# Performance work log

Measured on AMD Instinct MI355X. Metric: run time of the kernel, lower is better.

## Reference

```python
import jax, jax.numpy as jnp
import numpy as np

B, L, D, H, NB = 8, 256, 128, 4, 2
HD = D // H
N_ITEMS, TIME_SPAN = 50000, 256
EPS = 1e-8
NEG = -(2.0 ** 32) + 1.0  # torch uses -2**32+1 padding value


def _ln(x, g, b):
    m = jnp.mean(x, -1, keepdims=True)
    v = jnp.mean((x - m) ** 2, -1, keepdims=True)
    return (x - m) / jnp.sqrt(v + EPS) * g + b


def setup_inputs() -> dict:
    ks = iter(jax.random.split(jax.random.key(0), 40))

    def nrm(shape, s=0.02):
        return jax.random.normal(next(ks), shape, jnp.float32) * s

    inp = {
        "user_ids": jax.random.randint(next(ks), (B,), 0, 1000),
        "log_seqs": jax.random.randint(next(ks), (B, L), 0, N_ITEMS + 1),
        "time_matrices": jax.random.randint(next(ks), (B, L, L), 0, TIME_SPAN + 1),
        "pos_seqs": jax.random.randint(next(ks), (B, L), 1, N_ITEMS + 1),
        "neg_seqs": jax.random.randint(next(ks), (B, L), 1, N_ITEMS + 1),
    }
    inp["item_emb"] = nrm((N_ITEMS + 1, D)).at[0].set(0.0)  # padding_idx=0
    inp["posK_emb"] = nrm((L, D))
    inp["posV_emb"] = nrm((L, D))
    inp["timeK_emb"] = nrm((TIME_SPAN + 1, D))
    inp["timeV_emb"] = nrm((TIME_SPAN + 1, D))
    inp["ln1_g"] = jnp.ones((NB, D)); inp["ln1_b"] = jnp.zeros((NB, D))
    inp["Wq"] = nrm((NB, D, D)); inp["bq"] = jnp.zeros((NB, D))
    inp["Wk"] = nrm((NB, D, D)); inp["bk"] = jnp.zeros((NB, D))
    inp["Wv"] = nrm((NB, D, D)); inp["bv"] = jnp.zeros((NB, D))
    inp["ln2_g"] = jnp.ones((NB, D)); inp["ln2_b"] = jnp.zeros((NB, D))
    inp["W1"] = nrm((NB, D, D)); inp["b1"] = jnp.zeros((NB, D))
    inp["W2"] = nrm((NB, D, D)); inp["b2"] = jnp.zeros((NB, D))
    inp["lnf_g"] = jnp.ones((D,)); inp["lnf_b"] = jnp.zeros((D,))
    return inp


def reference(user_ids, log_seqs, time_matrices, pos_seqs, neg_seqs,
              item_emb, posK_emb, posV_emb, timeK_emb, timeV_emb,
              ln1_g, ln1_b, Wq, bq, Wk, bk, Wv, bv, ln2_g, ln2_b,
              W1, b1, W2, b2, lnf_g, lnf_b):
    # dropout layers are identity in eval mode
    seqs = item_emb[log_seqs] * jnp.sqrt(jnp.float32(D))          # [B,L,D]
    tK = timeK_emb[time_matrices].reshape(B, L, L, H, HD)          # [B,Lq,Lk,H,hd]
    tV = timeV_emb[time_matrices].reshape(B, L, L, H, HD)
    pad = log_seqs == 0                                            # [B,L]
    seqs = seqs * (~pad)[..., None]
    causal = jnp.triu(jnp.ones((L, L), bool), 1)                   # ~tril -> masked
    # time_mask masks by QUERY position (matches torch unsqueeze(-1).expand)
    mask = pad[:, None, :, None] | causal[None, None]              # [B,1,Lq,Lk]
    posKh = posK_emb.reshape(L, H, HD)
    posVh = posV_emb.reshape(L, H, HD)
    for i in range(NB):
        q_in = _ln(seqs, ln1_g[i], ln1_b[i])
        Qh = (q_in @ Wq[i] + bq[i]).reshape(B, L, H, HD).transpose(0, 2, 1, 3)
        Kh = (seqs @ Wk[i] + bk[i]).reshape(B, L, H, HD).transpose(0, 2, 1, 3)
        Vh = (seqs @ Wv[i] + bv[i]).reshape(B, L, H, HD).transpose(0, 2, 1, 3)
        scores = jnp.einsum("bhqd,bhkd->bhqk", Qh, Kh)
        scores = scores + jnp.einsum("bhqd,khd->bhqk", Qh, posKh)
        scores = scores + jnp.einsum("bqkhd,bhqd->bhqk", tK, Qh)
        scores = scores / jnp.sqrt(jnp.float32(HD))
        scores = jnp.where(mask, NEG, scores)
        A = jax.nn.softmax(scores, axis=-1)                        # [B,H,Lq,Lk]
        out = jnp.einsum("bhqk,bhkd->bhqd", A, Vh)
        out = out + jnp.einsum("bhqk,khd->bhqd", A, posVh)
        out = out + jnp.einsum("bhqk,bqkhd->bhqd", A, tV)
        out = out.transpose(0, 2, 1, 3).reshape(B, L, D)
        seqs = q_in + out                                          # residual on Q
        seqs = _ln(seqs, ln2_g[i], ln2_b[i])
        h = jax.nn.relu(seqs @ W1[i] + b1[i])                      # conv1d k=1 == linear
        seqs = seqs + (h @ W2[i] + b2[i])
        seqs = seqs * (~pad)[..., None]
    feats = _ln(seqs, lnf_g, lnf_b)
    pos_logits = jnp.sum(feats * item_emb[pos_seqs], -1)           # [B,L]
    neg_logits = jnp.sum(feats * item_emb[neg_seqs], -1)
    return (pos_logits, neg_logits)
```

## Files before the change

kernel.cpp:

```cpp
#include <hip/hip_runtime.h>
#include <hip/hip_bf16.h>

#define L_ 256
#define H_ 4
#define ROWS 2048
#define NEGV (-4294967295.0f)

typedef unsigned short us16;

__device__ __forceinline__ float us2f(us16 u){ return __uint_as_float(((unsigned)u)<<16); }
__device__ __forceinline__ us16 f2us(float f){ __hip_bfloat16 h=__float2bfloat16(f); return *(us16*)&h; }

__device__ __forceinline__ float dot2bf(unsigned x, unsigned y, float c){
#if __has_builtin(__builtin_amdgcn_fdot2_f32_bf16)
    typedef __bf16 bf2 __attribute__((ext_vector_type(2)));
    union U{ unsigned u; bf2 v; };
    U ux, uy; ux.u=x; uy.u=y;
    return __builtin_amdgcn_fdot2_f32_bf16(ux.v, uy.v, c, false);
#else
    float r=fmaf(us2f((us16)(x&0xffffu)), us2f((us16)(y&0xffffu)), c);
    return fmaf(us2f((us16)(x>>16)), us2f((us16)(y>>16)), r);
#endif
}

struct KArgs {
    const int *log_seqs, *tmat, *pos_seqs, *neg_seqs;
    const float *item_emb, *posK, *posV, *timeK, *timeV;
    const float *ln1g, *ln1b, *bq, *bk, *bv, *ln2g, *ln2b, *b1, *b2, *lnfg, *lnfb;
    const float *Wq, *Wk, *Wv, *W1, *W2;
    float *qin0, *qin1, *out;
    unsigned *wsP;
    us16 *tmK, *tmV, *Qb0, *Kb0, *Vb0, *Qb1, *Kb1, *Vb1;
};

__device__ __forceinline__ void ln_rows(float* sA,
        const float* __restrict__ g, const float* __restrict__ b,
        float* qin_out, int r0, int tid){
    int r=tid>>5, l=tid&31;
    float* x=sA+r*128;
    float x0=x[l],x1=x[l+32],x2=x[l+64],x3=x[l+96];
    float s=x0+x1+x2+x3;
    #pragma unroll
    for(int o=16;o;o>>=1) s+=__shfl_xor(s,o,64);
    float m=s*(1.f/128.f);
    float d0=x0-m,d1=x1-m,d2=x2-m,d3=x3-m;
    float v=d0*d0+d1*d1+d2*d2+d3*d3;
    #pragma unroll
    for(int o=16;o;o>>=1) v+=__shfl_xor(v,o,64);
    float rstd=rsqrtf(v*(1.f/128.f)+1e-8f);
    float y0=d0*rstd*g[l]+b[l];
    float y1=d1*rstd*g[l+32]+b[l+32];
    float y2=d2*rstd*g[l+64]+b[l+64];
    float y3=d3*rstd*g[l+96]+b[l+96];
    x[l]=y0; x[l+32]=y1; x[l+64]=y2; x[l+96]=y3;
    if(qin_out){
        float* q=qin_out+(size_t)(r0+r)*128;
        q[l]=y0; q[l+32]=y1; q[l+64]=y2; q[l+96]=y3;
    }
}

__device__ __forceinline__ float gemv128(const unsigned* __restrict__ wp,
                                         const unsigned* __restrict__ xp, int c){
    float s0=0.f, s1=0.f;
    #pragma unroll 8
    for(int kp=0;kp<64;kp+=2){
        s0=dot2bf(xp[kp],   wp[kp*128+c],     s0);
        s1=dot2bf(xp[kp+1], wp[(kp+1)*128+c], s1);
    }
    return s0+s1;
}

__global__ __launch_bounds__(256) void k_pre(KArgs a){
    __shared__ __align__(16) float sA[1024];
    int tid=threadIdx.x, bid=blockIdx.x;
    if(bid<768){
        int m=bid>>8, rg=bid&255, r0=rg*8;
        {
            int rl=tid>>5, c4=tid&31;
            int id=a.log_seqs[r0+rl];
            float4 v=((const float4*)a.item_emb)[id*32+c4];
            float sc = id? 11.3137085f : 0.f;
            v.x*=sc; v.y*=sc; v.z*=sc; v.w*=sc;
            ((float4*)sA)[tid]=v;
        }
        __syncthreads();
        if(m==0){ ln_rows(sA, a.ln1g, a.ln1b, a.qin0, r0, tid); __syncthreads(); }
        const float* Wsrc=(m==0)?a.Wq:(m==1)?a.Wk:a.Wv;
        int cp=tid&63, rp=tid>>6, c0=2*cp, ra=2*rp, rb=ra+1;
        float a00=0,a01=0,a10=0,a11=0;
        const float* Ar=sA+ra*128;
        const float* Br=sA+rb*128;
        #pragma unroll 8
        for(int kk=0;kk<128;kk++){
            float2 wp=((const float2*)(Wsrc+(size_t)kk*128))[cp];
            float x0=Ar[kk], x1=Br[kk];
            a00=fmaf(x0,wp.x,a00); a01=fmaf(x0,wp.y,a01);
            a10=fmaf(x1,wp.x,a10); a11=fmaf(x1,wp.y,a11);
        }
        int r_a=r0+ra, r_b=r0+rb;
        if(m==0){
            float b0v=a.bq[c0], b1v=a.bq[c0+1];
            ushort2 s0; s0.x=f2us(a00+b0v); s0.y=f2us(a01+b1v);
            ushort2 s1; s1.x=f2us(a10+b0v); s1.y=f2us(a11+b1v);
            *(ushort2*)(a.Qb0+(size_t)r_a*128+c0)=s0;
            *(ushort2*)(a.Qb0+(size_t)r_b*128+c0)=s1;
        } else if(m==1){
            float b0v=a.bk[c0], b1v=a.bk[c0+1];
            int qa=r_a&255, qb2=r_b&255;
            ushort2 s0; s0.x=f2us(a00+b0v+a.posK[qa*128+c0]);  s0.y=f2us(a01+b1v+a.posK[qa*128+c0+1]);
            ushort2 s1; s1.x=f2us(a10+b0v+a.posK[qb2*128+c0]); s1.y=f2us(a11+b1v+a.posK[qb2*128+c0+1]);
            *(ushort2*)(a.Kb0+(size_t)r_a*128+c0)=s0;
            *(ushort2*)(a.Kb0+(size_t)r_b*128+c0)=s1;
        } else {
            float b0v=a.bv[c0], b1v=a.bv[c0+1];
            int qa=r_a&255, qb2=r_b&255;
            unsigned lo0=f2us(a00+b0v+a.posV[qa*128+c0]);
            unsigned lo1=f2us(a01+b1v+a.posV[qa*128+c0+1]);
            unsigned hi0=f2us(a10+b0v+a.posV[qb2*128+c0]);
            unsigned hi1=f2us(a11+b1v+a.posV[qb2*128+c0+1]);
            unsigned* Vo=(unsigned*)a.Vb0+((size_t)r_a>>1)*128;
            Vo[c0]  =lo0|(hi0<<16);
            Vo[c0+1]=lo1|(hi1<<16);
        }
    } else if(bid<880){
        int j=bid-768; int m=j>>4; int sub=j&15;
        const float* base;
        switch(m){
            case 0: base=a.W1; break;        case 1: base=a.W2; break;
            case 2: base=a.Wq+16384; break;  case 3: base=a.Wk+16384; break;
            case 4: base=a.Wv+16384; break;  case 5: base=a.W1+16384; break;
            default: base=a.W2+16384; break;
        }
        unsigned* dst=a.wsP+(size_t)m*8192;
        #pragma unroll
        for(int t2=0;t2<2;t2++){
            int o=sub*512+t2*256+tid;
            int kp=o>>7, c=o&127;
            unsigned lo=f2us(base[(size_t)(2*kp)*128+c]);
            unsigned hi=f2us(base[(size_t)(2*kp+1)*128+c]);
            dst[o]=lo|(hi<<16);
        }
    } else {
        int gi=(bid-880)*256+tid;
        if(gi<8224){
            float4 v=((const float4*)a.timeK)[gi];
            ushort4 o; o.x=f2us(v.x);o.y=f2us(v.y);o.z=f2us(v.z);o.w=f2us(v.w);
            ((ushort4*)a.tmK)[gi]=o;
        } else if(gi<16448){
            int g2=gi-8224;
            float4 v=((const float4*)a.timeV)[g2];
            ushort4 o; o.x=f2us(v.x);o.y=f2us(v.y);o.z=f2us(v.z);o.w=f2us(v.w);
            ((ushort4*)a.tmV)[g2]=o;
        }
    }
}

__global__ __launch_bounds__(256,4) void k_blk(KArgs a, int layer){
    __shared__ __align__(16) float    sS[8*256];
    __shared__ __align__(16) unsigned sAb[8*128];
    __shared__ __align__(16) unsigned sQb[128];
    __shared__ __align__(16) int      sTM[512];
    __shared__ __align__(16) float    sPr[16*128];
    __shared__ float sRed[4], sRed2[4], sRB[8];
    __shared__ __align__(16) float    sX[256];
    __shared__ __align__(16) unsigned sXb[128];
    __shared__ __align__(16) unsigned sHb[128];
    __shared__ __align__(16) unsigned sYb[128];

    int tid=threadIdx.x, bid=blockIdx.x;
    int b=bid>>7, p=bid&127;
    int q1=p, q2=255-p, b0=b*L_;
    int r1=b0+q1, r2=b0+q2;
    bool pad1=a.log_seqs[r1]==0, pad2=a.log_seqs[r2]==0;
    const us16* Qb = layer? a.Qb1:a.Qb0;
    const us16* Kb = layer? a.Kb1:a.Kb0;
    const unsigned* Vbu = (const unsigned*)(layer? a.Vb1:a.Vb0);
    const float* qin = layer? a.qin1:a.qin0;
    const float scale=0.17677669529663687f;

    if(tid<128){
        int rowq=tid>>6, j=tid&63;
        int r=rowq?r2:r1;
        sQb[rowq*64+j]=((const unsigned*)Qb)[(size_t)r*64+j];
    }
    int k=tid;
    int tm1=a.tmat[(size_t)r1*L_+k], tm2=a.tmat[(size_t)r2*L_+k];
    sTM[k]=tm1; sTM[256+k]=tm2;
    __syncthreads();

    {
        const uint4* K4=(const uint4*)(Kb+(size_t)(b0+k)*128);
        #pragma unroll
        for(int i2=0;i2<2;i2++){
            int qq=i2?q2:q1; bool pad=i2?pad2:pad1;
            int tm=i2?tm2:tm1;
            bool act=(k<=qq)&&!pad;
            float acc[4]={0.f,0.f,0.f,0.f};
            if(act){
                const uint4* T4=(const uint4*)(a.tmK+(size_t)tm*128);
                const uint4* Q4=(const uint4*)(sQb+i2*64);
                #pragma unroll
                for(int c=0;c<16;c++){
                    uint4 kv=K4[c], tv=T4[c], qv=Q4[c];
                    float t=acc[c>>2];
                    t=dot2bf(qv.x,kv.x,t); t=dot2bf(qv.y,kv.y,t);
                    t=dot2bf(qv.z,kv.z,t); t=dot2bf(qv.w,kv.w,t);
                    t=dot2bf(qv.x,tv.x,t); t=dot2bf(qv.y,tv.y,t);
                    t=dot2bf(qv.z,tv.z,t); t=dot2bf(qv.w,tv.w,t);
                    acc[c>>2]=t;
                }
            }
            #pragma unroll
            for(int h2=0;h2<H_;h2++) sS[(i2*4+h2)*256+k]= act? acc[h2]*scale : NEGV;
        }
    }
    __syncthreads();

    {
        int h=tid>>6, lane=tid&63;
        us16* sab=(us16*)sAb;
        #pragma unroll
        for(int i2=0;i2<2;i2++){
            const float* row=sS+(i2*4+h)*256;
            float v0=row[lane],v1=row[lane+64],v2=row[lane+128],v3=row[lane+192];
            float mm=fmaxf(fmaxf(v0,v1),fmaxf(v2,v3));
            #pragma unroll
            for(int o=32;o;o>>=1) mm=fmaxf(mm,__shfl_xor(mm,o,64));
            float e0=__expf(v0-mm),e1=__expf(v1-mm),e2=__expf(v2-mm),e3=__expf(v3-mm);
            float ss=e0+e1+e2+e3;
            #pragma unroll
            for(int o=32;o;o>>=1) ss+=__shfl_xor(ss,o,64);
            float inv=1.f/ss;
            us16* ar=sab+(i2*4+h)*256;
            ar[lane]    =f2us(e0*inv); ar[lane+64] =f2us(e1*inv);
            ar[lane+128]=f2us(e2*inv); ar[lane+192]=f2us(e3*inv);
        }
    }
    __syncthreads();

    {
        int i2=tid>>7, s8=(tid>>4)&7, dq=tid&15;
        int qq=i2?q2:q1; bool pad=i2?pad2:pad1;
        int kend=pad?L_:qq+1;
        int k0=s8*32;
        int kmax=kend-k0; kmax=kmax<0?0:(kmax>32?32:kmax);
        int npair=(kmax+1)>>1;
        const unsigned* arow=sAb+(i2*4+(dq>>2))*128;
        const int* tmrow=sTM+i2*256;
        float ac0=0,ac1=0,ac2=0,ac3=0,ac4=0,ac5=0,ac6=0,ac7=0;
        for(int kp=0;kp<npair;kp++){
            int kx=k0+2*kp;
            unsigned aa=arow[kx>>1];
            int tma=tmrow[kx], tmb=tmrow[kx+1];
            const uint4* Vp=(const uint4*)(Vbu+((size_t)(b0+kx)>>1)*128+dq*8);
            uint4 va=Vp[0], vb4=Vp[1];
            uint4 ta=((const uint4*)(a.tmV+(size_t)tma*128))[dq];
            uint4 tb=((const uint4*)(a.tmV+(size_t)tmb*128))[dq];
            ac0=dot2bf(aa,va.x,ac0);  ac1=dot2bf(aa,va.y,ac1);
            ac2=dot2bf(aa,va.z,ac2);  ac3=dot2bf(aa,va.w,ac3);
            ac4=dot2bf(aa,vb4.x,ac4); ac5=dot2bf(aa,vb4.y,ac5);
            ac6=dot2bf(aa,vb4.z,ac6); ac7=dot2bf(aa,vb4.w,ac7);
            unsigned p0=__builtin_amdgcn_perm(tb.x,ta.x,0x05040100u);
            unsigned p1=__builtin_amdgcn_perm(tb.x,ta.x,0x07060302u);
            unsigned p2=__builtin_amdgcn_perm(tb.y,ta.y,0x05040100u);
            unsigned p3=__builtin_amdgcn_perm(tb.y,ta.y,0x07060302u);
            unsigned p4=__builtin_amdgcn_perm(tb.z,ta.z,0x05040100u);
            unsigned p5=__builtin_amdgcn_perm(tb.z,ta.z,0x07060302u);
            unsigned p6=__builtin_amdgcn_perm(tb.w,ta.w,0x05040100u);
            unsigned p7=__builtin_amdgcn_perm(tb.w,ta.w,0x07060302u);
            ac0=dot2bf(aa,p0,ac0); ac1=dot2bf(aa,p1,ac1);
            ac2=dot2bf(aa,p2,ac2); ac3=dot2bf(aa,p3,ac3);
            ac4=dot2bf(aa,p4,ac4); ac5=dot2bf(aa,p5,ac5);
            ac6=dot2bf(aa,p6,ac6); ac7=dot2bf(aa,p7,ac7);
        }
        float* dst=sPr+(i2*8+s8)*128+dq*8;
        ((float4*)dst)[0]=make_float4(ac0,ac1,ac2,ac3);
        ((float4*)dst)[1]=make_float4(ac4,ac5,ac6,ac7);
    }
    __syncthreads();

    int ii=tid>>7, l=tid&127;
    bool padown = ii? pad2:pad1;
    int rr = ii? r2:r1;
    int qown = ii? q2:q1;
    {
        float v=qin[(size_t)rr*128+l];
        #pragma unroll
        for(int sl=0;sl<8;sl++) v+=sPr[(ii*8+sl)*128+l];
        float s=v;
        #pragma unroll
        for(int o=32;o;o>>=1) s+=__shfl_xor(s,o,64);
        if((tid&63)==0) sRed[ii*2+((tid>>6)&1)]=s;
        __syncthreads();
        float m=(sRed[ii*2]+sRed[ii*2+1])*(1.f/128.f);
        float d=v-m;
        float vv=d*d;
        #pragma unroll
        for(int o=32;o;o>>=1) vv+=__shfl_xor(vv,o,64);
        if((tid&63)==0) sRed2[ii*2+((tid>>6)&1)]=vv;
        __syncthreads();
        float rstd=rsqrtf((sRed2[ii*2]+sRed2[ii*2+1])*(1.f/128.f)+1e-8f);
        float y=d*rstd*a.ln2g[layer*128+l]+a.ln2b[layer*128+l];
        sX[ii*128+l]=y;
        ((us16*)sXb)[ii*128+l]=f2us(y);
    }
    __syncthreads();

    int cc=l;
    {
        const unsigned* W1p=a.wsP+(size_t)(layer?5:0)*8192;
        float h1=gemv128(W1p, sXb+ii*64, cc);
        h1=fmaxf(h1+a.b1[layer*128+cc],0.f);
        ((us16*)sHb)[ii*128+cc]=f2us(h1);
    }
    __syncthreads();
    float f;
    {
        const unsigned* W2p=a.wsP+(size_t)(layer?6:1)*8192;
        f=gemv128(W2p, sHb+ii*64, cc)+a.b2[layer*128+cc]+sX[ii*128+cc];
        if(padown) f=0.f;
    }

    if(layer==0){
        ((us16*)sYb)[ii*128+cc]=f2us(f);
        float s=f;
        #pragma unroll
        for(int o=32;o;o>>=1) s+=__shfl_xor(s,o,64);
        if((tid&63)==0) sRB[ii*2+((tid>>6)&1)]=s;
        __syncthreads();
        float m=(sRB[ii*2]+sRB[ii*2+1])*(1.f/128.f);
        float d=f-m;
        float vv=d*d;
        #pragma unroll
        for(int o=32;o;o>>=1) vv+=__shfl_xor(vv,o,64);
        if((tid&63)==0) sRB[4+ii*2+((tid>>6)&1)]=vv;
        __syncthreads();
        float rstd=rsqrtf((sRB[4+ii*2]+sRB[5+ii*2])*(1.f/128.f)+1e-8f);
        float y1=d*rstd*a.ln1g[128+cc]+a.ln1b[128+cc];
        a.qin1[(size_t)rr*128+cc]=y1;
        ((us16*)sXb)[ii*128+cc]=f2us(y1);
        __syncthreads();
        float accq=gemv128(a.wsP+(size_t)2*8192, sXb+ii*64, cc)+a.bq[128+cc];
        a.Qb1[(size_t)rr*128+cc]=f2us(accq);
        float acck=gemv128(a.wsP+(size_t)3*8192, sYb+ii*64, cc)+a.bk[128+cc]+a.posK[qown*128+cc];
        a.Kb1[(size_t)rr*128+cc]=f2us(acck);
        float accv=gemv128(a.wsP+(size_t)4*8192, sYb+ii*64, cc)+a.bv[128+cc]+a.posV[qown*128+cc];
        ((us16*)a.Vb1)[((size_t)rr>>1)*256+2*cc+(rr&1)]=f2us(accv);
    } else {
        float s=f;
        #pragma unroll
        for(int o=32;o;o>>=1) s+=__shfl_xor(s,o,64);
        if((tid&63)==0) sRB[ii*2+((tid>>6)&1)]=s;
        __syncthreads();
        float m=(sRB[ii*2]+sRB[ii*2+1])*(1.f/128.f);
        float d=f-m;
        float vv=d*d;
        #pragma unroll
        for(int o=32;o;o>>=1) vv+=__shfl_xor(vv,o,64);
        if((tid&63)==0) sRB[4+ii*2+((tid>>6)&1)]=vv;
        __syncthreads();
        float rstd=rsqrtf((sRB[4+ii*2]+sRB[5+ii*2])*(1.f/128.f)+1e-8f);
        sX[ii*128+cc]=d*rstd*a.lnfg[cc]+a.lnfb[cc];
        __syncthreads();
        int w=tid>>6, lane=tid&63;
        int rowi=w>>1, neg=w&1;
        int rg = rowi? r2:r1;
        int id = neg? a.neg_seqs[rg] : a.pos_seqs[rg];
        const float* e=a.item_emb+(size_t)id*128;
        float s2 = sX[rowi*128+lane]*e[lane] + sX[rowi*128+lane+64]*e[lane+64];
        #pragma unroll
        for(int o=32;o;o>>=1) s2+=__shfl_xor(s2,o,64);
        if(lane==0) a.out[neg*ROWS+rg]=s2;
    }
}

extern "C" void kernel_launch(void* const* d_in, const int* in_sizes, int n_in,
                              void* d_out, int out_size, void* d_ws, size_t ws_size,
                              hipStream_t stream) {
    KArgs a;
    a.log_seqs=(const int*)d_in[1];
    a.tmat    =(const int*)d_in[2];
    a.pos_seqs=(const int*)d_in[3];
    a.neg_seqs=(const int*)d_in[4];
    a.item_emb=(const float*)d_in[5];
    a.posK =(const float*)d_in[6];
    a.posV =(const float*)d_in[7];
    a.timeK=(const float*)d_in[8];
    a.timeV=(const float*)d_in[9];
    a.ln1g=(const float*)d_in[10];
    a.ln1b=(const float*)d_in[11];
    a.Wq=(const float*)d_in[12];
    a.bq=(const float*)d_in[13];
    a.Wk=(const float*)d_in[14];
    a.bk=(const float*)d_in[15];
    a.Wv=(const float*)d_in[16];
    a.bv=(const float*)d_in[17];
    a.ln2g=(const float*)d_in[18];
    a.ln2b=(const float*)d_in[19];
    a.W1=(const float*)d_in[20];
    a.b1=(const float*)d_in[21];
    a.W2=(const float*)d_in[22];
    a.b2=(const float*)d_in[23];
    a.lnfg=(const float*)d_in[24];
    a.lnfb=(const float*)d_in[25];

    const size_t MB=1u<<20;
    char* w=(char*)d_ws;
    a.qin0=(float*)(w+0*MB);
    a.qin1=(float*)(w+1*MB);
    a.Qb0 =(us16*) (w+2*MB);
    a.Kb0 =(us16*) (w+2*MB+512*1024);
    a.Vb0 =(us16*) (w+3*MB);
    a.Qb1 =(us16*) (w+3*MB+512*1024);
    a.Kb1 =(us16*) (w+4*MB);
    a.Vb1 =(us16*) (w+4*MB+512*1024);
    a.wsP =(unsigned*)(w+5*MB);
    a.tmK =(us16*) (w+5*MB+256*1024);
    a.tmV =(us16*) (w+5*MB+384*1024);
    a.out =(float*)d_out;

    k_pre<<<946,256,0,stream>>>(a);
    k_blk<<<1024,256,0,stream>>>(a,0);
    k_blk<<<1024,256,0,stream>>>(a,1);
}
```

Baseline: 203.0 us.

## Precompute query-time-embedding projections and double block threads to 512

The kernel now precomputes Q·timeK dot products for all 257 time buckets once per block. Per-key scoring then looks up this table instead of streaming a timeK row per key, which removes most of the time-embedding gather traffic from the score phase. The block grows from 256 to 512 threads: the PV accumulation is split into 16 key slices and the FFN and projection GEMVs are split over K into halves reduced through shared memory. Shared buffers are aliased into a union to keep LDS usage down. In exchange the kernel has more barriers and idle half-blocks in the layer-norm phases, and 512 threads with launch bounds of 4 blocks may limit registers.

```diff
diff --git a/kernel.cpp b/kernel.cpp
--- a/kernel.cpp
+++ b/kernel.cpp
@@ -32,6 +32,18 @@
     unsigned *wsP;
     us16 *tmK, *tmV, *Qb0, *Kb0, *Vb0, *Qb1, *Kb1, *Vb1;
 };
+
+__device__ __forceinline__ float gemv32(const unsigned* __restrict__ wp,
+                                        const unsigned* __restrict__ xp, int c, int hk){
+    float s0=0.f, s1=0.f;
+    int base=hk*32;
+    #pragma unroll 8
+    for(int j=0;j<32;j+=2){
+        s0=dot2bf(xp[base+j],   wp[(size_t)(base+j)*128+c],   s0);
+        s1=dot2bf(xp[base+j+1], wp[(size_t)(base+j+1)*128+c], s1);
+    }
+    return s0+s1;
+}
 
 __device__ __forceinline__ void ln_rows(float* sA,
         const float* __restrict__ g, const float* __restrict__ b,
@@ -57,17 +69,6 @@
         float* q=qin_out+(size_t)(r0+r)*128;
         q[l]=y0; q[l+32]=y1; q[l+64]=y2; q[l+96]=y3;
     }
-}
-
-__device__ __forceinline__ float gemv128(const unsigned* __restrict__ wp,
-                                         const unsigned* __restrict__ xp, int c){
-    float s0=0.f, s1=0.f;
-    #pragma unroll 8
-    for(int kp=0;kp<64;kp+=2){
-        s0=dot2bf(xp[kp],   wp[kp*128+c],     s0);
-        s1=dot2bf(xp[kp+1], wp[(kp+1)*128+c], s1);
-    }
-    return s0+s1;
 }
 
 __global__ __launch_bounds__(256) void k_pre(KArgs a){
@@ -155,17 +156,21 @@
     }
 }
 
-__global__ __launch_bounds__(256,4) void k_blk(KArgs a, int layer){
-    __shared__ __align__(16) float    sS[8*256];
+__global__ __launch_bounds__(512,4) void k_blk(KArgs a, int layer){
+    __shared__ __align__(16) char uni[16448];
     __shared__ __align__(16) unsigned sAb[8*128];
+    __shared__ __align__(16) int      sTM[512];
     __shared__ __align__(16) unsigned sQb[128];
-    __shared__ __align__(16) int      sTM[512];
-    __shared__ __align__(16) float    sPr[16*128];
-    __shared__ float sRed[4], sRed2[4], sRB[8];
     __shared__ __align__(16) float    sX[256];
     __shared__ __align__(16) unsigned sXb[128];
     __shared__ __align__(16) unsigned sHb[128];
     __shared__ __align__(16) unsigned sYb[128];
+    __shared__ float sRed[4], sRed2[4], sRB[8];
+    float* sS =(float*)uni;
+    float* sPj=(float*)(uni+8192);
+    float* sPr=(float*)uni;
+    float* sG0=(float*)uni;
+    float* sG1=(float*)(uni+2048);
 
     int tid=threadIdx.x, bid=blockIdx.x;
     int b=bid>>7, p=bid&127;
@@ -183,67 +188,90 @@
         int r=rowq?r2:r1;
         sQb[rowq*64+j]=((const unsigned*)Qb)[(size_t)r*64+j];
     }
-    int k=tid;
-    int tm1=a.tmat[(size_t)r1*L_+k], tm2=a.tmat[(size_t)r2*L_+k];
-    sTM[k]=tm1; sTM[256+k]=tm2;
+    if(tid<256) sTM[tid]=a.tmat[(size_t)r1*L_+tid];
+    else        sTM[tid]=a.tmat[(size_t)r2*L_+(tid-256)];
     __syncthreads();
 
     {
+        int ch=tid&15, h=ch>>2;
+        uint4 qv0=((const uint4*)(sQb))[ch];
+        uint4 qv1=((const uint4*)(sQb+64))[ch];
+        for(int t=tid>>4; t<257; t+=32){
+            uint4 tv=((const uint4*)(a.tmK+(size_t)t*128))[ch];
+            float p0=0.f,p1=0.f;
+            p0=dot2bf(qv0.x,tv.x,p0); p0=dot2bf(qv0.y,tv.y,p0);
+            p0=dot2bf(qv0.z,tv.z,p0); p0=dot2bf(qv0.w,tv.w,p0);
+            p1=dot2bf(qv1.x,tv.x,p1); p1=dot2bf(qv1.y,tv.y,p1);
+            p1=dot2bf(qv1.z,tv.z,p1); p1=dot2bf(qv1.w,tv.w,p1);
+            p0+=__shfl_xor(p0,1,64); p0+=__shfl_xor(p0,2,64);
+            p1+=__shfl_xor(p1,1,64); p1+=__shfl_xor(p1,2,64);
+            if((ch&3)==0){
+                sPj[t*4+h]       =p0;
+                sPj[1028+t*4+h]  =p1;
+            }
+        }
+    }
+    __syncthreads();
+
+    {
+        int k=tid&255, i2=tid>>8;
         const uint4* K4=(const uint4*)(Kb+(size_t)(b0+k)*128);
-        #pragma unroll
-        for(int i2=0;i2<2;i2++){
-            int qq=i2?q2:q1; bool pad=i2?pad2:pad1;
-            int tm=i2?tm2:tm1;
-            bool act=(k<=qq)&&!pad;
-            float acc[4]={0.f,0.f,0.f,0.f};
-            if(act){
-                const uint4* T4=(const uint4*)(a.tmK+(size_t)tm*128);
-                const uint4* Q4=(const uint4*)(sQb+i2*64);
-                #pragma unroll
-                for(int c=0;c<16;c++){
-                    uint4 kv=K4[c], tv=T4[c], qv=Q4[c];
-                    float t=acc[c>>2];
-                    t=dot2bf(qv.x,kv.x,t); t=dot2bf(qv.y,kv.y,t);
-                    t=dot2bf(qv.z,kv.z,t); t=dot2bf(qv.w,kv.w,t);
-                    t=dot2bf(qv.x,tv.x,t); t=dot2bf(qv.y,tv.y,t);
-                    t=dot2bf(qv.z,tv.z,t); t=dot2bf(qv.w,tv.w,t);
-                    acc[c>>2]=t;
-                }
+        int qq=i2?q2:q1; bool pad=i2?pad2:pad1;
+        int tm=sTM[i2*256+k];
+        bool act=(k<=qq)&&!pad;
+        float o0=NEGV,o1=NEGV,o2=NEGV,o3=NEGV;
+        if(act){
+            const uint4* Q4=(const uint4*)(sQb+i2*64);
+            float4 pj=((const float4*)sPj)[i2*257+tm];
+            float r4[4];
+            #pragma unroll
+            for(int h=0;h<4;h++){
+                uint4 k0=K4[h*4+0],k1=K4[h*4+1],k2=K4[h*4+2],k3=K4[h*4+3];
+                uint4 qa=Q4[h*4+0],qb=Q4[h*4+1],qc=Q4[h*4+2],qd=Q4[h*4+3];
+                float s0=0,s1=0;
+                s0=dot2bf(qa.x,k0.x,s0); s1=dot2bf(qa.y,k0.y,s1);
+                s0=dot2bf(qa.z,k0.z,s0); s1=dot2bf(qa.w,k0.w,s1);
+                s0=dot2bf(qb.x,k1.x,s0); s1=dot2bf(qb.y,k1.y,s1);
+                s0=dot2bf(qb.z,k1.z,s0); s1=dot2bf(qb.w,k1.w,s1);
+                s0=dot2bf(qc.x,k2.x,s0); s1=dot2bf(qc.y,k2.y,s1);
+                s0=dot2bf(qc.z,k2.z,s0); s1=dot2bf(qc.w,k2.w,s1);
+                s0=dot2bf(qd.x,k3.x,s0); s1=dot2bf(qd.y,k3.y,s1);
+                s0=dot2bf(qd.z,k3.z,s0); s1=dot2bf(qd.w,k3.w,s1);
+                r4[h]=s0+s1;
             }
-            #pragma unroll
-            for(int h2=0;h2<H_;h2++) sS[(i2*4+h2)*256+k]= act? acc[h2]*scale : NEGV;
-        }
+            o0=(r4[0]+pj.x)*scale; o1=(r4[1]+pj.y)*scale;
+            o2=(r4[2]+pj.z)*scale; o3=(r4[3]+pj.w)*scale;
+        }
+        sS[(i2*4+0)*256+k]=o0; sS[(i2*4+1)*256+k]=o1;
+        sS[(i2*4+2)*256+k]=o2; sS[(i2*4+3)*256+k]=o3;
     }
     __syncthreads();
 
     {
-        int h=tid>>6, lane=tid&63;
-        us16* sab=(us16*)sAb;
-        #pragma unroll
-        for(int i2=0;i2<2;i2++){
-            const float* row=sS+(i2*4+h)*256;
-            float v0=row[lane],v1=row[lane+64],v2=row[lane+128],v3=row[lane+192];
-            float mm=fmaxf(fmaxf(v0,v1),fmaxf(v2,v3));
-            #pragma unroll
-            for(int o=32;o;o>>=1) mm=fmaxf(mm,__shfl_xor(mm,o,64));
-            float e0=__expf(v0-mm),e1=__expf(v1-mm),e2=__expf(v2-mm),e3=__expf(v3-mm);
-            float ss=e0+e1+e2+e3;
-            #pragma unroll
-            for(int o=32;o;o>>=1) ss+=__shfl_xor(ss,o,64);
-            float inv=1.f/ss;
-            us16* ar=sab+(i2*4+h)*256;
-            ar[lane]    =f2us(e0*inv); ar[lane+64] =f2us(e1*inv);
-            ar[lane+128]=f2us(e2*inv); ar[lane+192]=f2us(e3*inv);
-        }
+        int w=tid>>6, lane=tid&63;
+        int i2=w>>2, h=w&3;
+        const float* row=sS+(i2*4+h)*256;
+        float v0=row[lane],v1=row[lane+64],v2=row[lane+128],v3=row[lane+192];
+        float mm=fmaxf(fmaxf(v0,v1),fmaxf(v2,v3));
+        #pragma unroll
+        for(int o=32;o;o>>=1) mm=fmaxf(mm,__shfl_xor(mm,o,64));
+        float e0=__expf(v0-mm),e1=__expf(v1-mm),e2=__expf(v2-mm),e3=__expf(v3-mm);
+        float ss=e0+e1+e2+e3;
+        #pragma unroll
+        for(int o=32;o;o>>=1) ss+=__shfl_xor(ss,o,64);
+        float inv=1.f/ss;
+        us16* ar=((us16*)sAb)+(i2*4+h)*256;
+        ar[lane]    =f2us(e0*inv); ar[lane+64] =f2us(e1*inv);
+        ar[lane+128]=f2us(e2*inv); ar[lane+192]=f2us(e3*inv);
     }
     __syncthreads();
 
     {
-        int i2=tid>>7, s8=(tid>>4)&7, dq=tid&15;
+        int i2=tid>>8, s8=(tid>>4)&15, dq=tid&15;
         int qq=i2?q2:q1; bool pad=i2?pad2:pad1;
         int kend=pad?L_:qq+1;
-        int k0=s8*32;
-        int kmax=kend-k0; kmax=kmax<0?0:(kmax>32?32:kmax);
+        int k0=s8*16;
+        int kmax=kend-k0; kmax=kmax<0?0:(kmax>16?16:kmax);
         int npair=(kmax+1)>>1;
         const unsigned* arow=sAb+(i2*4+(dq>>2))*128;
         const int* tmrow=sTM+i2*256;
@@ -273,104 +301,130 @@
             ac4=dot2bf(aa,p4,ac4); ac5=dot2bf(aa,p5,ac5);
             ac6=dot2bf(aa,p6,ac6); ac7=dot2bf(aa,p7,ac7);
         }
-        float* dst=sPr+(i2*8+s8)*128+dq*8;
+        float* dst=sPr+(i2*16+s8)*128+dq*8;
         ((float4*)dst)[0]=make_float4(ac0,ac1,ac2,ac3);
         ((float4*)dst)[1]=make_float4(ac4,ac5,ac6,ac7);
     }
     __syncthreads();
 
-    int ii=tid>>7, l=tid&127;
-    bool padown = ii? pad2:pad1;
-    int rr = ii? r2:r1;
-    int qown = ii? q2:q1;
-    {
-        float v=qin[(size_t)rr*128+l];
-        #pragma unroll
-        for(int sl=0;sl<8;sl++) v+=sPr[(ii*8+sl)*128+l];
+    int ii=tid>>7&1, l=tid&127;
+    float v=0.f, d2v=0.f;
+    if(tid<256){
+        v=qin[(size_t)(ii?r2:r1)*128+l];
+        #pragma unroll
+        for(int sl=0;sl<16;sl++) v+=sPr[(ii*16+sl)*128+l];
         float s=v;
         #pragma unroll
         for(int o=32;o;o>>=1) s+=__shfl_xor(s,o,64);
         if((tid&63)==0) sRed[ii*2+((tid>>6)&1)]=s;
-        __syncthreads();
+    }
+    __syncthreads();
+    if(tid<256){
         float m=(sRed[ii*2]+sRed[ii*2+1])*(1.f/128.f);
-        float d=v-m;
-        float vv=d*d;
+        d2v=v-m;
+        float vv=d2v*d2v;
         #pragma unroll
         for(int o=32;o;o>>=1) vv+=__shfl_xor(vv,o,64);
         if((tid&63)==0) sRed2[ii*2+((tid>>6)&1)]=vv;
-        __syncthreads();
+    }
+    __syncthreads();
+    if(tid<256){
         float rstd=rsqrtf((sRed2[ii*2]+sRed2[ii*2+1])*(1.f/128.f)+1e-8f);
-        float y=d*rstd*a.ln2g[layer*128+l]+a.ln2b[layer*128+l];
+        float y=d2v*rstd*a.ln2g[layer*128+l]+a.ln2b[layer*128+l];
         sX[ii*128+l]=y;
         ((us16*)sXb)[ii*128+l]=f2us(y);
     }
     __syncthreads();
 
-    int cc=l;
-    {
-        const unsigned* W1p=a.wsP+(size_t)(layer?5:0)*8192;
-        float h1=gemv128(W1p, sXb+ii*64, cc);
-        h1=fmaxf(h1+a.b1[layer*128+cc],0.f);
-        ((us16*)sHb)[ii*128+cc]=f2us(h1);
-    }
-    __syncthreads();
-    float f;
-    {
-        const unsigned* W2p=a.wsP+(size_t)(layer?6:1)*8192;
-        f=gemv128(W2p, sHb+ii*64, cc)+a.b2[layer*128+cc]+sX[ii*128+cc];
-        if(padown) f=0.f;
+    int c=tid&127, iw=(tid>>7)&1, hk=tid>>8;
+    bool padw = iw? pad2:pad1;
+    int  rrw  = iw? r2:r1;
+    int  qw   = iw? q2:q1;
+    sG0[tid]=gemv32(a.wsP+(size_t)(layer?5:0)*8192, sXb+iw*64, c, hk);
+    __syncthreads();
+    if(hk==0){
+        float h1=sG0[tid]+sG0[tid+256]+a.b1[layer*128+c];
+        ((us16*)sHb)[iw*128+c]=f2us(fmaxf(h1,0.f));
+    }
+    __syncthreads();
+    sG1[tid]=gemv32(a.wsP+(size_t)(layer?6:1)*8192, sHb+iw*64, c, hk);
+    __syncthreads();
+    float f=0.f;
+    if(hk==0){
+        f=sG1[tid]+sG1[tid+256]+a.b2[layer*128+c]+sX[iw*128+c];
+        if(padw) f=0.f;
     }
 
     if(layer==0){
-        ((us16*)sYb)[ii*128+cc]=f2us(f);
-        float s=f;
-        #pragma unroll
-        for(int o=32;o;o>>=1) s+=__shfl_xor(s,o,64);
-        if((tid&63)==0) sRB[ii*2+((tid>>6)&1)]=s;
-        __syncthreads();
-        float m=(sRB[ii*2]+sRB[ii*2+1])*(1.f/128.f);
-        float d=f-m;
-        float vv=d*d;
-        #pragma unroll
-        for(int o=32;o;o>>=1) vv+=__shfl_xor(vv,o,64);
-        if((tid&63)==0) sRB[4+ii*2+((tid>>6)&1)]=vv;
-        __syncthreads();
-        float rstd=rsqrtf((sRB[4+ii*2]+sRB[5+ii*2])*(1.f/128.f)+1e-8f);
-        float y1=d*rstd*a.ln1g[128+cc]+a.ln1b[128+cc];
-        a.qin1[(size_t)rr*128+cc]=y1;
-        ((us16*)sXb)[ii*128+cc]=f2us(y1);
-        __syncthreads();
-        float accq=gemv128(a.wsP+(size_t)2*8192, sXb+ii*64, cc)+a.bq[128+cc];
-        a.Qb1[(size_t)rr*128+cc]=f2us(accq);
-        float acck=gemv128(a.wsP+(size_t)3*8192, sYb+ii*64, cc)+a.bk[128+cc]+a.posK[qown*128+cc];
-        a.Kb1[(size_t)rr*128+cc]=f2us(acck);
-        float accv=gemv128(a.wsP+(size_t)4*8192, sYb+ii*64, cc)+a.bv[128+cc]+a.posV[qown*128+cc];
-        ((us16*)a.Vb1)[((size_t)rr>>1)*256+2*cc+(rr&1)]=f2us(accv);
+        float d=0.f;
+        if(hk==0){
+            ((us16*)sYb)[iw*128+c]=f2us(f);
+            float s=f;
+            #pragma unroll
+            for(int o=32;o;o>>=1) s+=__shfl_xor(s,o,64);
+            if((tid&63)==0) sRB[iw*2+((tid>>6)&1)]=s;
+        }
+        __syncthreads();
+        if(hk==0){
+            float m=(sRB[iw*2]+sRB[iw*2+1])*(1.f/128.f);
+            d=f-m;
+            float vv=d*d;
+            #pragma unroll
+            for(int o=32;o;o>>=1) vv+=__shfl_xor(vv,o,64);
+            if((tid&63)==0) sRB[4+iw*2+((tid>>6)&1)]=vv;
+        }
+        __syncthreads();
+        if(hk==0){
+            float rstd=rsqrtf((sRB[4+iw*2]+sRB[5+iw*2])*(1.f/128.f)+1e-8f);
+            float y1=d*rstd*a.ln1g[128+c]+a.ln1b[128+c];
+            a.qin1[(size_t)rrw*128+c]=y1;
+            ((us16*)sXb)[iw*128+c]=f2us(y1);
+        }
+        __syncthreads();
+        sG0[tid]=gemv32(a.wsP+(size_t)2*8192, sXb+iw*64, c, hk);
+        __syncthreads();
+        if(hk==0) a.Qb1[(size_t)rrw*128+c]=f2us(sG0[tid]+sG0[tid+256]+a.bq[128+c]);
+        sG1[tid]=gemv32(a.wsP+(size_t)3*8192, sYb+iw*64, c, hk);
+        __syncthreads();
+        if(hk==0) a.Kb1[(size_t)rrw*128+c]=f2us(sG1[tid]+sG1[tid+256]+a.bk[128+c]+a.posK[qw*128+c]);
+        sG0[tid]=gemv32(a.wsP+(size_t)4*8192, sYb+iw*64, c, hk);
+        __syncthreads();
+        if(hk==0) ((us16*)a.Vb1)[((size_t)rrw>>1)*256+2*c+(rrw&1)]
+                    =f2us(sG0[tid]+sG0[tid+256]+a.bv[128+c]+a.posV[qw*128+c]);
     } else {
-        float s=f;
-        #pragma unroll
-        for(int o=32;o;o>>=1) s+=__shfl_xor(s,o,64);
-        if((tid&63)==0) sRB[ii*2+((tid>>6)&1)]=s;
-        __syncthreads();
-        float m=(sRB[ii*2]+sRB[ii*2+1])*(1.f/128.f);
-        float d=f-m;
-        float vv=d*d;
-        #pragma unroll
-        for(int o=32;o;o>>=1) vv+=__shfl_xor(vv,o,64);
-        if((tid&63)==0) sRB[4+ii*2+((tid>>6)&1)]=vv;
-        __syncthreads();
-        float rstd=rsqrtf((sRB[4+ii*2]+sRB[5+ii*2])*(1.f/128.f)+1e-8f);
-        sX[ii*128+cc]=d*rstd*a.lnfg[cc]+a.lnfb[cc];
+        float d=0.f;
+        if(hk==0){
+            float s=f;
+            #pragma unroll
+            for(int o=32;o;o>>=1) s+=__shfl_xor(s,o,64);
+            if((tid&63)==0) sRB[iw*2+((tid>>6)&1)]=s;
+        }
+        __syncthreads();
+        if(hk==0){
+            float m=(sRB[iw*2]+sRB[iw*2+1])*(1.f/128.f);
+            d=f-m;
+            float vv=d*d;
+            #pragma unroll
+            for(int o=32;o;o>>=1) vv+=__shfl_xor(vv,o,64);
+            if((tid&63)==0) sRB[4+iw*2+((tid>>6)&1)]=vv;
+        }
+        __syncthreads();
+        if(hk==0){
+            float rstd=rsqrtf((sRB[4+iw*2]+sRB[5+iw*2])*(1.f/128.f)+1e-8f);
+            sX[iw*128+c]=d*rstd*a.lnfg[c]+a.lnfb[c];
+        }
         __syncthreads();
         int w=tid>>6, lane=tid&63;
-        int rowi=w>>1, neg=w&1;
-        int rg = rowi? r2:r1;
-        int id = neg? a.neg_seqs[rg] : a.pos_seqs[rg];
-        const float* e=a.item_emb+(size_t)id*128;
-        float s2 = sX[rowi*128+lane]*e[lane] + sX[rowi*128+lane+64]*e[lane+64];
-        #pragma unroll
-        for(int o=32;o;o>>=1) s2+=__shfl_xor(s2,o,64);
-        if(lane==0) a.out[neg*ROWS+rg]=s2;
+        if(w<4){
+            int rowi=w>>1, neg=w&1;
+            int rg = rowi? r2:r1;
+            int id = neg? a.neg_seqs[rg] : a.pos_seqs[rg];
+            const float* e=a.item_emb+(size_t)id*128;
+            float s2 = sX[rowi*128+lane]*e[lane] + sX[rowi*128+lane+64]*e[lane+64];
+            #pragma unroll
+            for(int o=32;o;o>>=1) s2+=__shfl_xor(s2,o,64);
+            if(lane==0) a.out[neg*ROWS+rg]=s2;
+        }
     }
 }
 
@@ -420,6 +474,6 @@
     a.out =(float*)d_out;
 
     k_pre<<<946,256,0,stream>>>(a);
-    k_blk<<<1024,256,0,stream>>>(a,0);
-    k_blk<<<1024,256,0,stream>>>(a,1);
-}
+    k_blk<<<1024,512,0,stream>>>(a,0);
+    k_blk<<<1024,512,0,stream>>>(a,1);
+}
```

New measurement: 206.6 us. No clear change (+1.8%).
